# Kernel tuning notes

Measured on AMD Instinct MI355X. Metric: run time of the kernel, lower is better.

## Reference

```python
import jax, jax.numpy as jnp
import numpy as np

NUM_LOCATIONS = 100000
EMBED_DIM = 256
NUM_CLUSTERS = 50
B, L = 64, 200


def setup_inputs() -> dict:
    key = jax.random.key(0)
    k0, k1, k2, k3, k4 = jax.random.split(key, 5)
    loc_ids = jax.random.randint(k0, (B, L), 0, NUM_LOCATIONS)
    # nn.Embedding(num_locations, D, padding_idx=0): row 0 is zeros
    loc_table = jax.random.normal(k1, (NUM_LOCATIONS, EMBED_DIM), dtype=jnp.float32) * 0.02
    loc_table = loc_table.at[0].set(0.0)
    cluster_table = jax.random.normal(k2, (NUM_CLUSTERS, EMBED_DIM // 2), dtype=jnp.float32) * 0.02
    # nn.Linear(num_locations, num_clusters): weight (C, V), bias (C,)
    W_lc = jax.random.normal(k3, (NUM_CLUSTERS, NUM_LOCATIONS), dtype=jnp.float32) * 0.01
    b_lc = jax.random.normal(k4, (NUM_CLUSTERS,), dtype=jnp.float32) * 0.01
    return {"loc_ids": loc_ids, "loc_table": loc_table, "cluster_table": cluster_table,
            "W_lc": W_lc, "b_lc": b_lc}


def reference(loc_ids, loc_table, cluster_table, W_lc, b_lc):
    # fine = embedding lookup: (B, L, D)
    fine = loc_table[loc_ids]
    # one_hot(loc_ids) @ W_lc.T + b_lc  ==  gather columns of W_lc + bias (exact same math)
    logits = W_lc.T[loc_ids] + b_lc            # (B, L, C)
    cluster_weights = jax.nn.softmax(logits, axis=-1)
    # coarse = softmax-weighted mixture of cluster embeddings: (B, L, D//2)
    coarse = jnp.einsum('blc,cd->bld', cluster_weights, cluster_table)
    return jnp.concatenate([fine, coarse], axis=-1)  # (B, L, D + D//2)
```

## Files before the change

### kernel.cpp

```cpp
#include <hip/hip_runtime.h>
#include <hip/hip_bf16.h>

#define NUM_LOC   100000
#define EMB_D     256
#define NCLUST    50
#define NTOK      12800
#define OUT_D     384

__global__ __launch_bounds__(256)
void hle_kernel(const int*   __restrict__ loc_ids,
                const float* __restrict__ loc_table,
                const float* __restrict__ cluster_table,
                const float* __restrict__ W_lc,
                const float* __restrict__ b_lc,
                float*       __restrict__ out)
{
    __shared__ float s_ct[NCLUST * 128];

    const int tid = threadIdx.x;

    {
        const float4* src = (const float4*)cluster_table;
        float4* dst = (float4*)s_ct;
        for (int i = tid; i < NCLUST * 32; i += 256)
            dst[i] = src[i];
    }
    __syncthreads();

    const int wave  = tid >> 6;
    const int lane  = tid & 63;
    const int token = blockIdx.x * 4 + wave;
    const int id    = loc_ids[token];

    const float4* fsrc = (const float4*)(loc_table + (size_t)id * EMB_D);
    float4 fine = fsrc[lane];

    float logit = -INFINITY;
    if (lane < NCLUST)
        logit = W_lc[(size_t)lane * NUM_LOC + id] + b_lc[lane];

    float m = logit;
    #pragma unroll
    for (int off = 32; off > 0; off >>= 1)
        m = fmaxf(m, __shfl_xor(m, off, 64));

    float e = (lane < NCLUST) ? __expf(logit - m) : 0.0f;

    float s = e;
    #pragma unroll
    for (int off = 32; off > 0; off >>= 1)
        s += __shfl_xor(s, off, 64);

    const float w = e / s;

    float acc0 = 0.0f, acc1 = 0.0f;
    const float2* ct2 = (const float2*)s_ct;
    #pragma unroll
    for (int c = 0; c < NCLUST; ++c) {
        float wc = __shfl(w, c, 64);
        float2 v = ct2[c * 64 + lane];
        acc0 = fmaf(wc, v.x, acc0);
        acc1 = fmaf(wc, v.y, acc1);
    }

    float* orow = out + (size_t)token * OUT_D;

    ((float4*)orow)[lane] = fine;

    float2 cw = make_float2(acc0, acc1);
    ((float2*)(orow + EMB_D))[lane] = cw;
}

extern "C" void kernel_launch(void* const* d_in, const int* in_sizes, int n_in,
                              void* d_out, int out_size, void* d_ws, size_t ws_size,
                              hipStream_t stream) {
    const int*   loc_ids       = (const int*)d_in[0];
    const float* loc_table     = (const float*)d_in[1];
    const float* cluster_table = (const float*)d_in[2];
    const float* W_lc          = (const float*)d_in[3];
    const float* b_lc          = (const float*)d_in[4];
    float*       out           = (float*)d_out;

    hle_kernel<<<NTOK / 4, 256, 0, stream>>>(loc_ids, loc_table, cluster_table,
                                             W_lc, b_lc, out);
}
```

Measured before the change: 170.9 us.

## Drop LDS staging of cluster table and use nontemporal loads/stores

Removes the per-block shared-memory copy of the cluster table and the barrier, reading cluster rows directly from global memory (cached in L1/L2), and partially unrolls that loop. Embedding-row loads and output stores become nontemporal to avoid polluting the cache, the W_lc gather is issued before the fine load, the token index is made wave-uniform, and the division becomes a fast reciprocal. The cost is repeated global/L2 reads of the 25 KB cluster table per wave instead of one shared copy per block, plus slightly lower precision in the softmax normalization.

```diff
diff --git a/kernel.cpp b/kernel.cpp
--- a/kernel.cpp
+++ b/kernel.cpp
@@ -1,11 +1,13 @@
 #include <hip/hip_runtime.h>
-#include <hip/hip_bf16.h>
 
 #define NUM_LOC   100000
 #define EMB_D     256
 #define NCLUST    50
 #define NTOK      12800
 #define OUT_D     384
+
+typedef float f32x4 __attribute__((ext_vector_type(4)));
+typedef float f32x2 __attribute__((ext_vector_type(2)));
 
 __global__ __launch_bounds__(256)
 void hle_kernel(const int*   __restrict__ loc_ids,
@@ -15,29 +17,18 @@
                 const float* __restrict__ b_lc,
                 float*       __restrict__ out)
 {
-    __shared__ float s_ct[NCLUST * 128];
-
-    const int tid = threadIdx.x;
-
-    {
-        const float4* src = (const float4*)cluster_table;
-        float4* dst = (float4*)s_ct;
-        for (int i = tid; i < NCLUST * 32; i += 256)
-            dst[i] = src[i];
-    }
-    __syncthreads();
-
+    const int tid   = threadIdx.x;
     const int wave  = tid >> 6;
     const int lane  = tid & 63;
-    const int token = blockIdx.x * 4 + wave;
+    const int token = __builtin_amdgcn_readfirstlane(blockIdx.x * 4 + wave);
     const int id    = loc_ids[token];
-
-    const float4* fsrc = (const float4*)(loc_table + (size_t)id * EMB_D);
-    float4 fine = fsrc[lane];
 
     float logit = -INFINITY;
     if (lane < NCLUST)
         logit = W_lc[(size_t)lane * NUM_LOC + id] + b_lc[lane];
+
+    const f32x4* fsrc = (const f32x4*)(loc_table + (size_t)id * EMB_D);
+    f32x4 fine = __builtin_nontemporal_load(fsrc + lane);
 
     float m = logit;
     #pragma unroll
@@ -51,24 +42,22 @@
     for (int off = 32; off > 0; off >>= 1)
         s += __shfl_xor(s, off, 64);
 
-    const float w = e / s;
+    const float w = e * __builtin_amdgcn_rcpf(s);
 
     float acc0 = 0.0f, acc1 = 0.0f;
-    const float2* ct2 = (const float2*)s_ct;
-    #pragma unroll
+    const f32x2* ct2 = (const f32x2*)cluster_table;
+    #pragma unroll 10
     for (int c = 0; c < NCLUST; ++c) {
         float wc = __shfl(w, c, 64);
-        float2 v = ct2[c * 64 + lane];
-        acc0 = fmaf(wc, v.x, acc0);
-        acc1 = fmaf(wc, v.y, acc1);
+        f32x2 v = ct2[c * 64 + lane];
+        acc0 = __builtin_fmaf(wc, v.x, acc0);
+        acc1 = __builtin_fmaf(wc, v.y, acc1);
     }
 
     float* orow = out + (size_t)token * OUT_D;
-
-    ((float4*)orow)[lane] = fine;
-
-    float2 cw = make_float2(acc0, acc1);
-    ((float2*)(orow + EMB_D))[lane] = cw;
+    __builtin_nontemporal_store(fine, (f32x4*)orow + lane);
+    f32x2 cw = { acc0, acc1 };
+    __builtin_nontemporal_store(cw, (f32x2*)(orow + EMB_D) + lane);
 }
 
 extern "C" void kernel_launch(void* const* d_in, const int* in_sizes, int n_in,
```

Result: slower. 175.4 us (+2.7%).
